# Performance work log

Hardware: AMD Instinct MI355X
Metric: run time of the kernel (lower is better)

## Reference

```python
import jax, jax.numpy as jnp
import numpy as np
from jax import lax

NUM_NODES = 100000
FEAT = 256
RANK = 16
NNZ = 4000000
NUM_HE = 125000  # num_hyperedges == num_edges_total
K = 2000000      # int(0.5 * NNZ)


def setup_inputs() -> dict:
    key = jax.random.key(0)
    ks = jax.random.split(key, 6)
    x = jax.random.normal(ks[0], (NUM_NODES, FEAT), dtype=jnp.float32)
    W = jax.random.normal(ks[1], (RANK, FEAT), dtype=jnp.float32)
    edge_factors = jax.random.normal(ks[2], (NUM_HE, RANK), dtype=jnp.float32)
    V_idx = jax.random.randint(ks[3], (NNZ,), 0, NUM_NODES, dtype=jnp.int32)
    E_idx = jax.random.randint(ks[4], (NNZ,), 0, NUM_HE, dtype=jnp.int32)
    edge_ids = jax.random.randint(ks[5], (NUM_HE,), 0, NUM_HE, dtype=jnp.int32)
    return {"x": x, "W": W, "edge_factors": edge_factors,
            "V_idx": V_idx, "E_idx": E_idx, "edge_ids": edge_ids, "k": K}


def _segment_mean(vals, seg_ids, num_segments):
    s = jax.ops.segment_sum(vals, seg_ids, num_segments=num_segments)
    c = jax.ops.segment_sum(jnp.ones_like(vals), seg_ids, num_segments=num_segments)
    return s / jnp.maximum(c, 1.0)


def reference(x, W, edge_factors, V_idx, E_idx, edge_ids, k):
    # node_proj(x): [N, rank]; gather per-incidence node and edge factors, dot product
    proj = x @ W.T                                  # [N, rank]
    ef = edge_factors[edge_ids[E_idx]]              # [nnz, rank]
    logits = jnp.sum(proj[V_idx] * ef, axis=-1)     # [nnz]
    scores = jax.nn.sigmoid(logits)

    # is_test=True path: deterministic top-k keep set
    _, keep_ids = lax.top_k(scores, k)
    hard = jnp.zeros_like(scores).at[keep_ids].set(1.0)
    # straight-through: forward == hard, gradient flows through scores where hard==1
    soft = hard + (scores - lax.stop_gradient(scores)) * hard

    edge_probs = _segment_mean(lax.stop_gradient(scores), E_idx, NUM_HE)
    edge_soft = _segment_mean(soft, E_idx, NUM_HE)
    edge_hard = (_segment_mean(hard, E_idx, NUM_HE) > 0).astype(jnp.float32)
    return scores, soft, hard, edge_probs, edge_soft, edge_hard
```

## Files before the change

### kernel.cpp

```cpp
#include <hip/hip_runtime.h>
#include <math.h>

#define FEAT 256
#define RANKK 16
#define PRJ_NODES 16
#define CAND_CAP 131072
#define TIE_CAP 2048
#define NBK_MAX 512

typedef unsigned long long u64;

static __device__ __forceinline__ u64 pack_pair(unsigned e_low, unsigned bits, unsigned idx) {
    return ((u64)e_low << 56) | ((u64)bits << 26) | (u64)idx;
}

__global__ __launch_bounds__(256) void proj_kernel(const float* __restrict__ x,
        const float* __restrict__ Wm, float* __restrict__ proj, int n_nodes) {
    __shared__ float Ws[RANKK][FEAT + 4];
    __shared__ float Xs[PRJ_NODES][FEAT + 4];
    const float4* x4 = (const float4*)x;
    const float4* w4 = (const float4*)Wm;
    for (int t = threadIdx.x; t < RANKK * (FEAT / 4); t += 256) {
        int r = t >> 6, j4 = t & 63;
        *(float4*)&Ws[r][j4 * 4] = w4[t];
    }
    int nodeBase = blockIdx.x * PRJ_NODES;
    for (int t = threadIdx.x; t < PRJ_NODES * (FEAT / 4); t += 256) {
        int n = t >> 6, j4 = t & 63;
        int node = nodeBase + n;
        float4 v = make_float4(0.f, 0.f, 0.f, 0.f);
        if (node < n_nodes) v = x4[(size_t)node * (FEAT / 4) + j4];
        *(float4*)&Xs[n][j4 * 4] = v;
    }
    __syncthreads();
    int n = threadIdx.x >> 4, r = threadIdx.x & 15;
    int node = nodeBase + n;
    if (node >= n_nodes) return;
    double acc = 0.0;
    #pragma unroll 8
    for (int j4 = 0; j4 < FEAT / 4; ++j4) {
        float4 xv = *(const float4*)&Xs[n][j4 * 4];
        float4 wv = *(const float4*)&Ws[r][j4 * 4];
        acc += (double)xv.x * (double)wv.x + (double)xv.y * (double)wv.y
             + (double)xv.z * (double)wv.z + (double)xv.w * (double)wv.w;
    }
    proj[(size_t)node * RANKK + r] = (float)acc;
}

__global__ void gather_ef(const float4* __restrict__ ef, const int* __restrict__ edge_ids,
                          float4* __restrict__ ef2, int nhe) {
    int t = blockIdx.x * blockDim.x + threadIdx.x;
    if (t >= nhe * 4) return;
    int e = t >> 2, c = t & 3;
    ef2[(size_t)e * 4 + c] = ef[(size_t)edge_ids[e] * 4 + c];
}

__global__ void ehist_kernel(const int* __restrict__ E_idx, unsigned* __restrict__ bucketCnt,
                             int nnz, int nb) {
    __shared__ unsigned h[NBK_MAX];
    for (int t = threadIdx.x; t < NBK_MAX; t += blockDim.x) h[t] = 0;
    __syncthreads();
    for (int i = blockIdx.x * blockDim.x + threadIdx.x; i < nnz; i += gridDim.x * blockDim.x)
        atomicAdd(&h[((unsigned)E_idx[i]) >> 8], 1u);
    __syncthreads();
    for (int t = threadIdx.x; t < nb; t += blockDim.x)
        if (h[t]) atomicAdd(&bucketCnt[t], h[t]);
}

__global__ void bucket_scan(const unsigned* __restrict__ bucketCnt,
                            unsigned* __restrict__ bucketBase, unsigned* __restrict__ cursor,
                            int nb, int nnz) {
    __shared__ unsigned s[NBK_MAX];
    int t = threadIdx.x;
    unsigned c = (t < nb) ? bucketCnt[t] : 0u;
    s[t] = c;
    __syncthreads();
    for (int off = 1; off < NBK_MAX; off <<= 1) {
        unsigned v = (t >= off) ? s[t - off] : 0u;
        __syncthreads();
        s[t] += v;
        __syncthreads();
    }
    unsigned excl = s[t] - c;
    if (t < nb) { bucketBase[t] = excl; cursor[t] = excl; }
    if (t == 0) bucketBase[nb] = (unsigned)nnz;
}

__global__ __launch_bounds__(256) void score_kernel(
        const float4* __restrict__ proj4, const float4* __restrict__ ef4,
        const int* __restrict__ V_idx, const int* __restrict__ E_idx,
        float* __restrict__ scores, int nnz) {
    int stride = gridDim.x * blockDim.x;
    #pragma unroll 2
    for (int i = blockIdx.x * blockDim.x + threadIdx.x; i < nnz; i += stride) {
        int v = V_idx[i], e = E_idx[i];
        float4 p0 = proj4[(size_t)v * 4 + 0];
        float4 p1 = proj4[(size_t)v * 4 + 1];
        float4 p2 = proj4[(size_t)v * 4 + 2];
        float4 p3 = proj4[(size_t)v * 4 + 3];
        float4 f0 = ef4[(size_t)e * 4 + 0];
        float4 f1 = ef4[(size_t)e * 4 + 1];
        float4 f2 = ef4[(size_t)e * 4 + 2];
        float4 f3 = ef4[(size_t)e * 4 + 3];
        double acc = (double)p0.x * f0.x + (double)p0.y * f0.y + (double)p0.z * f0.z + (double)p0.w * f0.w
                   + (double)p1.x * f1.x + (double)p1.y * f1.y + (double)p1.z * f1.z + (double)p1.w * f1.w
                   + (double)p2.x * f2.x + (double)p2.y * f2.y + (double)p2.z * f2.z + (double)p2.w * f2.w
                   + (double)p3.x * f3.x + (double)p3.y * f3.y + (double)p3.z * f3.z + (double)p3.w * f3.w;
        scores[i] = (float)(1.0 / (1.0 + exp(-acc)));
    }
}

__global__ void hist1_kernel(const float4* __restrict__ scores4, unsigned* __restrict__ hist1g,
                             int n4, int nnz) {
    __shared__ unsigned h[4096];
    for (int t = threadIdx.x; t < 4096; t += blockDim.x) h[t] = 0;
    __syncthreads();
    unsigned r1016 = 0, r1015 = 0, r0 = 0;
    int stride = gridDim.x * blockDim.x;
    for (int i = blockIdx.x * blockDim.x + threadIdx.x; i < n4; i += stride) {
        float4 sv = scores4[i];
        unsigned bb[4] = {__float_as_uint(sv.x), __float_as_uint(sv.y),
                          __float_as_uint(sv.z), __float_as_uint(sv.w)};
        #pragma unroll
        for (int q = 0; q < 4; ++q) {
            unsigned b = bb[q] >> 20;
            if (b == 1016) ++r1016;
            else if (b == 1015) ++r1015;
            else if (b == 0) ++r0;
            else atomicAdd(&h[b], 1u);
        }
    }
    for (int i = n4 * 4 + blockIdx.x * blockDim.x + threadIdx.x; i < nnz; i += stride) {
        unsigned b = __float_as_uint(((const float*)scores4)[i]) >> 20;
        if (b == 1016) ++r1016;
        else if (b == 1015) ++r1015;
        else if (b == 0) ++r0;
        else atomicAdd(&h[b], 1u);
    }
    if (r1016) atomicAdd(&h[1016], r1016);
    if (r1015) atomicAdd(&h[1015], r1015);
    if (r0) atomicAdd(&h[0], r0);
    __syncthreads();
    for (int t = threadIdx.x; t < 4096; t += blockDim.x)
        if (h[t]) atomicAdd(&hist1g[t], h[t]);
}

#define PB_CHUNK 8192
__global__ __launch_bounds__(256) void pair_build(const int* __restrict__ E_idx,
        const float* __restrict__ scores, u64* __restrict__ pairs,
        unsigned* __restrict__ cursor, int nnz, int nb) {
    __shared__ unsigned bh[NBK_MAX];
    for (int t = threadIdx.x; t < NBK_MAX; t += 256) bh[t] = 0;
    __syncthreads();
    int base = blockIdx.x * PB_CHUNK;
    int nE = nnz - base;
    if (nE > PB_CHUNK) nE = PB_CHUNK;
    for (int o = threadIdx.x; o < nE; o += 256)
        atomicAdd(&bh[((unsigned)E_idx[base + o]) >> 8], 1u);
    __syncthreads();
    for (int b = threadIdx.x; b < nb; b += 256) {
        unsigned c = bh[b];
        bh[b] = c ? atomicAdd(&cursor[b], c) : 0u;
    }
    __syncthreads();
    for (int o = threadIdx.x; o < nE; o += 256) {
        int i = base + o;
        unsigned e = (unsigned)E_idx[i];
        unsigned bits = __float_as_uint(scores[i]);
        unsigned pos = atomicAdd(&bh[e >> 8], 1u);
        pairs[pos] = pack_pair(e & 255u, bits, (unsigned)i);
    }
}

__global__ void scan1_kernel(const unsigned* __restrict__ hist,
                             unsigned* __restrict__ sel, const int* __restrict__ kptr) {
    __shared__ unsigned sfx[256];
    int t = threadIdx.x;
    unsigned local[16];
    unsigned s = 0;
    #pragma unroll
    for (int j = 0; j < 16; ++j) { local[j] = hist[t * 16 + j]; s += local[j]; }
    sfx[t] = s;
    __syncthreads();
    for (int off = 1; off < 256; off <<= 1) {
        unsigned add = (t + off < 256) ? sfx[t + off] : 0;
        __syncthreads();
        sfx[t] += add;
        __syncthreads();
    }
    unsigned krem = (unsigned)(*kptr);
    unsigned above = (t + 1 < 256) ? sfx[t + 1] : 0;
    if (above < krem && sfx[t] >= krem) {
        unsigned cum = above;
        int b = t * 16;
        for (int j = 15; j >= 0; --j) {
            unsigned cc = local[j];
            if (cum + cc >= krem) { b = t * 16 + j; break; }
            cum += cc;
        }
        sel[0] = krem - cum;
        sel[1] = ((unsigned)b) << 20;
    }
}

__global__ void compact_kernel(const u64* __restrict__ pairs, const unsigned* __restrict__ sel,
                               uint2* __restrict__ cand, unsigned* __restrict__ candCount, int nnz) {
    unsigned pref = sel[1] >> 20;
    int tid = blockIdx.x * blockDim.x + threadIdx.x;
    int stride = gridDim.x * blockDim.x;
    int lane = threadIdx.x & 63;
    for (int i = tid; i < nnz; i += stride) {
        u64 p = pairs[i];
        unsigned bits = (unsigned)(p >> 26) & 0x3FFFFFFFu;
        bool pred = (bits >> 20) == pref;
        unsigned long long mask = __ballot(pred);
        if (mask) {
            int leader = __ffsll(mask) - 1;
            unsigned base = 0;
            if (lane == leader) base = atomicAdd(candCount, (unsigned)__popcll(mask));
            base = __shfl(base, leader, 64);
            if (pred) {
                unsigned rank = __popcll(mask & ((1ull << lane) - 1ull));
                unsigned pos = base + rank;
                if (pos < CAND_CAP) cand[pos] = make_uint2(bits, (unsigned)(p & 0x3FFFFFFu));
            }
        }
    }
}

__global__ __launch_bounds__(256) void select_small(const uint2* __restrict__ cand,
                            const unsigned* __restrict__ candCount,
                            unsigned* __restrict__ sel, unsigned* __restrict__ tieList) {
    __shared__ unsigned h2[4096];
    __shared__ unsigned sfx[256];
    __shared__ unsigned sB2, sKrem2, sT, sM;
    __shared__ unsigned h3[256];
    __shared__ unsigned ties[TIE_CAP];
    __shared__ unsigned tcnt;
    int t = threadIdx.x;
    unsigned nc = *candCount;
    int n = (nc < CAND_CAP) ? (int)nc : CAND_CAP;
    unsigned krem = sel[0];
    unsigned pref = sel[1];

    for (int j = t; j < 4096; j += 256) h2[j] = 0;
    if (t == 0) tcnt = 0;
    __syncthreads();
    for (int j = t; j < n; j += 256) atomicAdd(&h2[(cand[j].x >> 8) & 0xFFF], 1u);
    __syncthreads();

    unsigned local[16];
    unsigned s = 0;
    #pragma unroll
    for (int j = 0; j < 16; ++j) { local[j] = h2[t * 16 + j]; s += local[j]; }
    sfx[t] = s;
    __syncthreads();
    for (int off = 1; off < 256; off <<= 1) {
        unsigned add = (t + off < 256) ? sfx[t + off] : 0;
        __syncthreads();
        sfx[t] += add;
        __syncthreads();
    }
    {
        unsigned above = (t + 1 < 256) ? sfx[t + 1] : 0;
        if (above < krem && sfx[t] >= krem) {
            unsigned cum = above;
            int b = t * 16;
            for (int j = 15; j >= 0; --j) {
                unsigned cc = local[j];
                if (cum + cc >= krem) { b = t * 16 + j; break; }
                cum += cc;
            }
            sB2 = (unsigned)b;
            sKrem2 = krem - cum;
        }
    }
    __syncthreads();

    h3[t] = 0;
    __syncthreads();
    unsigned b2 = sB2;
    for (int j = t; j < n; j += 256) {
        unsigned x = cand[j].x;
        if (((x >> 8) & 0xFFF) == b2) atomicAdd(&h3[x & 0xFF], 1u);
    }
    __syncthreads();
    sfx[t] = h3[t];
    __syncthreads();
    for (int off = 1; off < 256; off <<= 1) {
        unsigned add = (t + off < 256) ? sfx[t + off] : 0;
        __syncthreads();
        sfx[t] += add;
        __syncthreads();
    }
    {
        unsigned krem2 = sKrem2;
        unsigned above = (t + 1 < 256) ? sfx[t + 1] : 0;
        if (above < krem2 && sfx[t] >= krem2) {
            sT = pref | (b2 << 8) | (unsigned)t;
            sM = krem2 - above;
        }
    }
    __syncthreads();

    unsigned T = sT;
    for (int j = t; j < n; j += 256) {
        if (cand[j].x == T) {
            unsigned p = atomicAdd(&tcnt, 1u);
            if (p < TIE_CAP) ties[p] = cand[j].y;
        }
    }
    __syncthreads();
    if (t == 0) {
        unsigned cnt = (tcnt < TIE_CAP) ? tcnt : TIE_CAP;
        for (unsigned a = 1; a < cnt; ++a) {
            unsigned key = ties[a];
            int bpos = (int)a - 1;
            while (bpos >= 0 && ties[bpos] > key) { ties[bpos + 1] = ties[bpos]; --bpos; }
            ties[bpos + 1] = key;
        }
        unsigned m = sM;
        if (m > cnt) m = cnt;
        sel[2] = T;
        sel[3] = m;
        for (unsigned j = 0; j < m; ++j) tieList[j] = ties[j];
    }
}

__global__ __launch_bounds__(256) void esum_kernel(const u64* __restrict__ pairs,
        const unsigned* __restrict__ bucketBase,
        float* __restrict__ e_ssum, unsigned* __restrict__ e_cnt, int nhe) {
    __shared__ float ss[256];
    __shared__ unsigned cc[256];
    int t = threadIdx.x, b = blockIdx.x;
    ss[t] = 0.f; cc[t] = 0u;
    __syncthreads();
    unsigned n0 = bucketBase[b], n1 = bucketBase[b + 1];
    for (unsigned j = n0 + t; j < n1; j += 256) {
        u64 p = pairs[j];
        unsigned el = (unsigned)(p >> 56);
        unsigned bits = (unsigned)(p >> 26) & 0x3FFFFFFFu;
        atomicAdd(&ss[el], __uint_as_float(bits));
        atomicAdd(&cc[el], 1u);
    }
    __syncthreads();
    int e = b * 256 + t;
    if (e < nhe) { e_ssum[e] = ss[t]; e_cnt[e] = cc[t]; }
}

__global__ __launch_bounds__(256) void ehard_kernel(const u64* __restrict__ pairs,
        const unsigned* __restrict__ bucketBase, const unsigned* __restrict__ sel,
        const unsigned* __restrict__ tieList, unsigned* __restrict__ e_hsum, int nhe) {
    __shared__ unsigned hh[256];
    __shared__ unsigned ties[TIE_CAP];
    unsigned T = sel[2];
    unsigned m = sel[3];
    if (m > TIE_CAP) m = TIE_CAP;
    hh[threadIdx.x] = 0;
    for (int j = threadIdx.x; j < (int)m; j += 256) ties[j] = tieList[j];
    __syncthreads();
    int b = blockIdx.x;
    unsigned n0 = bucketBase[b], n1 = bucketBase[b + 1];
    for (unsigned j = n0 + threadIdx.x; j < n1; j += 256) {
        u64 p = pairs[j];
        unsigned bits = (unsigned)(p >> 26) & 0x3FFFFFFFu;
        bool keep = bits > T;
        if (bits == T) {
            unsigned idx = (unsigned)(p & 0x3FFFFFFu);
            int lo = 0, hi = (int)m - 1;
            keep = false;
            while (lo <= hi) {
                int mid = (lo + hi) >> 1;
                unsigned v = ties[mid];
                if (v == idx) { keep = true; break; }
                if (v < idx) lo = mid + 1; else hi = mid - 1;
            }
        }
        if (keep) atomicAdd(&hh[(unsigned)(p >> 56)], 1u);
    }
    __syncthreads();
    int e = b * 256 + threadIdx.x;
    if (e < nhe) e_hsum[e] = hh[threadIdx.x];
}

__global__ __launch_bounds__(256) void write_hard(const float4* __restrict__ scores4,
                           const unsigned* __restrict__ sel,
                           const unsigned* __restrict__ tieList,
                           float4* __restrict__ hard4, float4* __restrict__ soft4,
                           int n4, int nnz) {
    __shared__ unsigned ties[TIE_CAP];
    unsigned T = sel[2];
    unsigned m = sel[3];
    if (m > TIE_CAP) m = TIE_CAP;
    for (int j = threadIdx.x; j < (int)m; j += blockDim.x) ties[j] = tieList[j];
    __syncthreads();
    int tid = blockIdx.x * blockDim.x + threadIdx.x;
    int stride = gridDim.x * blockDim.x;
    for (int i = tid; i < n4; i += stride) {
        float4 sv = scores4[i];
        unsigned bb[4] = {__float_as_uint(sv.x), __float_as_uint(sv.y),
                          __float_as_uint(sv.z), __float_as_uint(sv.w)};
        float hv[4];
        #pragma unroll
        for (int q = 0; q < 4; ++q) {
            bool keep = (bb[q] > T);
            if (bb[q] == T) {
                unsigned idx = (unsigned)(i * 4 + q);
                int lo = 0, hi = (int)m - 1;
                keep = false;
                while (lo <= hi) {
                    int mid = (lo + hi) >> 1;
                    unsigned v = ties[mid];
                    if (v == idx) { keep = true; break; }
                    if (v < idx) lo = mid + 1; else hi = mid - 1;
                }
            }
            hv[q] = keep ? 1.0f : 0.0f;
        }
        float4 outv = make_float4(hv[0], hv[1], hv[2], hv[3]);
        hard4[i] = outv;
        soft4[i] = outv;
    }
    const float* sc = (const float*)scores4;
    float* hard = (float*)hard4;
    float* soft = (float*)soft4;
    for (int i = n4 * 4 + tid; i < nnz; i += stride) {
        unsigned b = __float_as_uint(sc[i]);
        bool keep = (b > T);
        if (b == T) {
            unsigned idx = (unsigned)i;
            int lo = 0, hi = (int)m - 1;
            keep = false;
            while (lo <= hi) {
                int mid = (lo + hi) >> 1;
                unsigned v = ties[mid];
                if (v == idx) { keep = true; break; }
                if (v < idx) lo = mid + 1; else hi = mid - 1;
            }
        }
        float hvv = keep ? 1.0f : 0.0f;
        hard[i] = hvv;
        soft[i] = hvv;
    }
}

__global__ void finalize_edges(const float* __restrict__ ssum, const unsigned* __restrict__ cnt,
                               const unsigned* __restrict__ hsum,
                               float* __restrict__ eprob, float* __restrict__ esoft,
                               float* __restrict__ ehard, int nhe) {
    int j = blockIdx.x * blockDim.x + threadIdx.x;
    if (j >= nhe) return;
    float c = fmaxf((float)cnt[j], 1.0f);
    eprob[j] = ssum[j] / c;
    esoft[j] = (float)hsum[j] / c;
    ehard[j] = (hsum[j] > 0) ? 1.0f : 0.0f;
}

extern "C" void kernel_launch(void* const* d_in, const int* in_sizes, int n_in,
                              void* d_out, int out_size, void* d_ws, size_t ws_size,
                              hipStream_t stream) {
    const float* x        = (const float*)d_in[0];
    const float* Wm       = (const float*)d_in[1];
    const float* ef       = (const float*)d_in[2];
    const int*   V_idx    = (const int*)d_in[3];
    const int*   E_idx    = (const int*)d_in[4];
    const int*   edge_ids = (const int*)d_in[5];
    const int*   kptr     = (const int*)d_in[6];

    const int nnz     = in_sizes[3];
    const int nhe     = in_sizes[5];
    const int n_nodes = in_sizes[0] / FEAT;
    const int nb      = (nhe + 255) >> 8;

    float* out    = (float*)d_out;
    float* scores = out;
    float* soft   = out + (size_t)nnz;
    float* hard   = out + 2 * (size_t)nnz;
    float* eprob  = out + 3 * (size_t)nnz;
    float* esoft  = eprob + nhe;
    float* ehard  = esoft + nhe;

    u64*   pairs = (u64*)soft;
    uint2* cand  = (uint2*)eprob;

    char* w = (char*)d_ws;
    unsigned* hist1      = (unsigned*)w;
    unsigned* bucketCnt  = hist1 + 4096;
    unsigned* candCount  = bucketCnt + NBK_MAX;
    unsigned* sel        = candCount + 1;
    unsigned* tieList    = sel + 8;
    unsigned* bucketBase = tieList + TIE_CAP;
    unsigned* cursor     = bucketBase + NBK_MAX + 1;
    float*    e_ssum     = (float*)(cursor + NBK_MAX);
    unsigned* e_cnt      = (unsigned*)(e_ssum + nhe);
    unsigned* e_hsum     = e_cnt + nhe;
    char* auxEnd = (char*)(e_hsum + nhe);
    size_t auxAligned = (((size_t)(auxEnd - w)) + 255) & ~(size_t)255;

    size_t ef2Bytes  = (size_t)nhe * RANKK * sizeof(float);
    size_t projBytes = (size_t)n_nodes * RANKK * sizeof(float);

    float* ef2;
    float* proj;
    if (ws_size >= auxAligned + ef2Bytes + projBytes) {
        ef2  = (float*)(w + auxAligned);
        proj = (float*)(w + auxAligned + ef2Bytes);
    } else {
        ef2  = hard;
        proj = hard + (size_t)nhe * RANKK;
    }

    hipMemsetAsync(w, 0, (size_t)(4096 + NBK_MAX + 1) * sizeof(unsigned), stream);

    ehist_kernel<<<128, 256, 0, stream>>>(E_idx, bucketCnt, nnz, nb);
    bucket_scan<<<1, NBK_MAX, 0, stream>>>(bucketCnt, bucketBase, cursor, nb, nnz);
    gather_ef<<<(nhe * 4 + 255) / 256, 256, 0, stream>>>(
        (const float4*)ef, edge_ids, (float4*)ef2, nhe);
    proj_kernel<<<(n_nodes + PRJ_NODES - 1) / PRJ_NODES, 256, 0, stream>>>(x, Wm, proj, n_nodes);

    score_kernel<<<2048, 256, 0, stream>>>(
        (const float4*)proj, (const float4*)ef2, V_idx, E_idx, scores, nnz);

    int n4 = nnz / 4;
    hist1_kernel<<<128, 256, 0, stream>>>((const float4*)scores, hist1, n4, nnz);
    pair_build<<<(nnz + PB_CHUNK - 1) / PB_CHUNK, 256, 0, stream>>>(
        E_idx, scores, pairs, cursor, nnz, nb);

    scan1_kernel<<<1, 256, 0, stream>>>(hist1, sel, kptr);
    compact_kernel<<<1024, 256, 0, stream>>>(pairs, sel, cand, candCount, nnz);
    select_small<<<1, 256, 0, stream>>>(cand, candCount, sel, tieList);

    esum_kernel<<<nb, 256, 0, stream>>>(pairs, bucketBase, e_ssum, e_cnt, nhe);
    ehard_kernel<<<nb, 256, 0, stream>>>(pairs, bucketBase, sel, tieList, e_hsum, nhe);

    write_hard<<<1024, 256, 0, stream>>>(
        (const float4*)scores, sel, tieList, (float4*)hard, (float4*)soft, n4, nnz);
    finalize_edges<<<(nhe + 255) / 256, 256, 0, stream>>>(e_ssum, e_cnt, e_hsum,
                                                          eprob, esoft, ehard, nhe);
}
```

Before: 525.6 us.

## Fuse histogram into scoring, compact from scores, merge edge reduction kernels

The score kernel now processes two incidences per thread via int2 index loads and builds the 4096-bin score histogram itself, so the separate hist1 pass over scores is gone. Compaction of candidates reads the 4-byte scores array with float4 loads instead of the 8-byte packed pairs. The three edge kernels (sum/count, hard count, finalize) become one kernel that reads the bucketed pairs once and writes the final edge outputs directly. This cuts global memory traffic and launch count. In exchange, every one of the 2048 score blocks now flushes its own shared histogram to global memory, and the score kernel uses more registers.

After: 539.8 us. +2.7%, slower.

```diff
diff --git a/kernel.cpp b/kernel.cpp
--- a/kernel.cpp
+++ b/kernel.cpp
@@ -88,60 +88,70 @@
 
 __global__ __launch_bounds__(256) void score_kernel(
         const float4* __restrict__ proj4, const float4* __restrict__ ef4,
-        const int* __restrict__ V_idx, const int* __restrict__ E_idx,
-        float* __restrict__ scores, int nnz) {
-    int stride = gridDim.x * blockDim.x;
-    #pragma unroll 2
-    for (int i = blockIdx.x * blockDim.x + threadIdx.x; i < nnz; i += stride) {
-        int v = V_idx[i], e = E_idx[i];
-        float4 p0 = proj4[(size_t)v * 4 + 0];
-        float4 p1 = proj4[(size_t)v * 4 + 1];
-        float4 p2 = proj4[(size_t)v * 4 + 2];
-        float4 p3 = proj4[(size_t)v * 4 + 3];
-        float4 f0 = ef4[(size_t)e * 4 + 0];
-        float4 f1 = ef4[(size_t)e * 4 + 1];
-        float4 f2 = ef4[(size_t)e * 4 + 2];
-        float4 f3 = ef4[(size_t)e * 4 + 3];
-        double acc = (double)p0.x * f0.x + (double)p0.y * f0.y + (double)p0.z * f0.z + (double)p0.w * f0.w
-                   + (double)p1.x * f1.x + (double)p1.y * f1.y + (double)p1.z * f1.z + (double)p1.w * f1.w
-                   + (double)p2.x * f2.x + (double)p2.y * f2.y + (double)p2.z * f2.z + (double)p2.w * f2.w
-                   + (double)p3.x * f3.x + (double)p3.y * f3.y + (double)p3.z * f3.z + (double)p3.w * f3.w;
-        scores[i] = (float)(1.0 / (1.0 + exp(-acc)));
-    }
-}
-
-__global__ void hist1_kernel(const float4* __restrict__ scores4, unsigned* __restrict__ hist1g,
-                             int n4, int nnz) {
+        const int2* __restrict__ V2, const int2* __restrict__ E2,
+        float2* __restrict__ scores2, unsigned* __restrict__ hist1g,
+        int npair, int nnz) {
     __shared__ unsigned h[4096];
-    for (int t = threadIdx.x; t < 4096; t += blockDim.x) h[t] = 0;
+    for (int t = threadIdx.x; t < 4096; t += 256) h[t] = 0;
     __syncthreads();
     unsigned r1016 = 0, r1015 = 0, r0 = 0;
-    int stride = gridDim.x * blockDim.x;
-    for (int i = blockIdx.x * blockDim.x + threadIdx.x; i < n4; i += stride) {
-        float4 sv = scores4[i];
-        unsigned bb[4] = {__float_as_uint(sv.x), __float_as_uint(sv.y),
-                          __float_as_uint(sv.z), __float_as_uint(sv.w)};
-        #pragma unroll
-        for (int q = 0; q < 4; ++q) {
-            unsigned b = bb[q] >> 20;
-            if (b == 1016) ++r1016;
-            else if (b == 1015) ++r1015;
-            else if (b == 0) ++r0;
-            else atomicAdd(&h[b], 1u);
-        }
-    }
-    for (int i = n4 * 4 + blockIdx.x * blockDim.x + threadIdx.x; i < nnz; i += stride) {
-        unsigned b = __float_as_uint(((const float*)scores4)[i]) >> 20;
-        if (b == 1016) ++r1016;
-        else if (b == 1015) ++r1015;
-        else if (b == 0) ++r0;
-        else atomicAdd(&h[b], 1u);
+    int stride = gridDim.x * 256;
+    for (int i = blockIdx.x * 256 + threadIdx.x; i < npair; i += stride) {
+        int2 v = V2[i];
+        int2 e = E2[i];
+        float4 a0 = proj4[(size_t)v.x * 4 + 0];
+        float4 a1 = proj4[(size_t)v.x * 4 + 1];
+        float4 a2 = proj4[(size_t)v.x * 4 + 2];
+        float4 a3 = proj4[(size_t)v.x * 4 + 3];
+        float4 b0 = proj4[(size_t)v.y * 4 + 0];
+        float4 b1 = proj4[(size_t)v.y * 4 + 1];
+        float4 b2 = proj4[(size_t)v.y * 4 + 2];
+        float4 b3 = proj4[(size_t)v.y * 4 + 3];
+        float4 f0 = ef4[(size_t)e.x * 4 + 0];
+        float4 f1 = ef4[(size_t)e.x * 4 + 1];
+        float4 f2 = ef4[(size_t)e.x * 4 + 2];
+        float4 f3 = ef4[(size_t)e.x * 4 + 3];
+        float4 g0 = ef4[(size_t)e.y * 4 + 0];
+        float4 g1 = ef4[(size_t)e.y * 4 + 1];
+        float4 g2 = ef4[(size_t)e.y * 4 + 2];
+        float4 g3 = ef4[(size_t)e.y * 4 + 3];
+        double acc0 = (double)a0.x * f0.x + (double)a0.y * f0.y + (double)a0.z * f0.z + (double)a0.w * f0.w
+                    + (double)a1.x * f1.x + (double)a1.y * f1.y + (double)a1.z * f1.z + (double)a1.w * f1.w
+                    + (double)a2.x * f2.x + (double)a2.y * f2.y + (double)a2.z * f2.z + (double)a2.w * f2.w
+                    + (double)a3.x * f3.x + (double)a3.y * f3.y + (double)a3.z * f3.z + (double)a3.w * f3.w;
+        double acc1 = (double)b0.x * g0.x + (double)b0.y * g0.y + (double)b0.z * g0.z + (double)b0.w * g0.w
+                    + (double)b1.x * g1.x + (double)b1.y * g1.y + (double)b1.z * g1.z + (double)b1.w * g1.w
+                    + (double)b2.x * g2.x + (double)b2.y * g2.y + (double)b2.z * g2.z + (double)b2.w * g2.w
+                    + (double)b3.x * g3.x + (double)b3.y * g3.y + (double)b3.z * g3.z + (double)b3.w * g3.w;
+        float s0 = (float)(1.0 / (1.0 + exp(-acc0)));
+        float s1 = (float)(1.0 / (1.0 + exp(-acc1)));
+        scores2[i] = make_float2(s0, s1);
+        unsigned bb0 = __float_as_uint(s0) >> 20;
+        unsigned bb1 = __float_as_uint(s1) >> 20;
+        if (bb0 == 1016) ++r1016; else if (bb0 == 1015) ++r1015;
+        else if (bb0 == 0) ++r0; else atomicAdd(&h[bb0], 1u);
+        if (bb1 == 1016) ++r1016; else if (bb1 == 1015) ++r1015;
+        else if (bb1 == 0) ++r0; else atomicAdd(&h[bb1], 1u);
+    }
+    if ((nnz & 1) && blockIdx.x == 0 && threadIdx.x == 0) {
+        int i = nnz - 1;
+        const int* Vi = (const int*)V2;
+        const int* Ei = (const int*)E2;
+        const float* pr = (const float*)proj4;
+        const float* fr = (const float*)ef4;
+        int v = Vi[i], e = Ei[i];
+        double acc = 0.0;
+        for (int r = 0; r < RANKK; ++r)
+            acc += (double)pr[(size_t)v * RANKK + r] * (double)fr[(size_t)e * RANKK + r];
+        float s = (float)(1.0 / (1.0 + exp(-acc)));
+        ((float*)scores2)[i] = s;
+        atomicAdd(&hist1g[__float_as_uint(s) >> 20], 1u);
     }
     if (r1016) atomicAdd(&h[1016], r1016);
     if (r1015) atomicAdd(&h[1015], r1015);
     if (r0) atomicAdd(&h[0], r0);
     __syncthreads();
-    for (int t = threadIdx.x; t < 4096; t += blockDim.x)
+    for (int t = threadIdx.x; t < 4096; t += 256)
         if (h[t]) atomicAdd(&hist1g[t], h[t]);
 }
 
@@ -203,27 +213,44 @@
     }
 }
 
-__global__ void compact_kernel(const u64* __restrict__ pairs, const unsigned* __restrict__ sel,
-                               uint2* __restrict__ cand, unsigned* __restrict__ candCount, int nnz) {
+__global__ void compact_kernel(const float4* __restrict__ scores4,
+                               const unsigned* __restrict__ sel,
+                               uint2* __restrict__ cand, unsigned* __restrict__ candCount,
+                               int n4, int nnz) {
     unsigned pref = sel[1] >> 20;
     int tid = blockIdx.x * blockDim.x + threadIdx.x;
     int stride = gridDim.x * blockDim.x;
     int lane = threadIdx.x & 63;
-    for (int i = tid; i < nnz; i += stride) {
-        u64 p = pairs[i];
-        unsigned bits = (unsigned)(p >> 26) & 0x3FFFFFFFu;
-        bool pred = (bits >> 20) == pref;
-        unsigned long long mask = __ballot(pred);
-        if (mask) {
-            int leader = __ffsll(mask) - 1;
-            unsigned base = 0;
-            if (lane == leader) base = atomicAdd(candCount, (unsigned)__popcll(mask));
-            base = __shfl(base, leader, 64);
-            if (pred) {
-                unsigned rank = __popcll(mask & ((1ull << lane) - 1ull));
-                unsigned pos = base + rank;
-                if (pos < CAND_CAP) cand[pos] = make_uint2(bits, (unsigned)(p & 0x3FFFFFFu));
+    int niter = (n4 + stride - 1) / stride;
+    for (int kk = 0; kk < niter; ++kk) {
+        int i = tid + kk * stride;
+        bool inb = (i < n4);
+        float4 sv = make_float4(0.f, 0.f, 0.f, 0.f);
+        if (inb) sv = scores4[i];
+        unsigned bb[4] = {__float_as_uint(sv.x), __float_as_uint(sv.y),
+                          __float_as_uint(sv.z), __float_as_uint(sv.w)};
+        #pragma unroll
+        for (int q = 0; q < 4; ++q) {
+            bool pred = inb && ((bb[q] >> 20) == pref);
+            unsigned long long mask = __ballot(pred);
+            if (mask) {
+                int leader = __ffsll(mask) - 1;
+                unsigned base = 0;
+                if (lane == leader) base = atomicAdd(candCount, (unsigned)__popcll(mask));
+                base = __shfl(base, leader, 64);
+                if (pred) {
+                    unsigned rank = __popcll(mask & ((1ull << lane) - 1ull));
+                    unsigned pos = base + rank;
+                    if (pos < CAND_CAP) cand[pos] = make_uint2(bb[q], (unsigned)(i * 4 + q));
+                }
             }
+        }
+    }
+    for (int i = n4 * 4 + tid; i < nnz; i += stride) {
+        unsigned b = __float_as_uint(((const float*)scores4)[i]);
+        if ((b >> 20) == pref) {
+            unsigned pos = atomicAdd(candCount, 1u);
+            if (pos < CAND_CAP) cand[pos] = make_uint2(b, (unsigned)i);
         }
     }
 }
@@ -327,14 +354,23 @@
     }
 }
 
-__global__ __launch_bounds__(256) void esum_kernel(const u64* __restrict__ pairs,
-        const unsigned* __restrict__ bucketBase,
-        float* __restrict__ e_ssum, unsigned* __restrict__ e_cnt, int nhe) {
+__global__ __launch_bounds__(256) void edge_final(const u64* __restrict__ pairs,
+        const unsigned* __restrict__ bucketBase, const unsigned* __restrict__ sel,
+        const unsigned* __restrict__ tieList,
+        float* __restrict__ eprob, float* __restrict__ esoft, float* __restrict__ ehard,
+        int nhe) {
     __shared__ float ss[256];
     __shared__ unsigned cc[256];
-    int t = threadIdx.x, b = blockIdx.x;
-    ss[t] = 0.f; cc[t] = 0u;
-    __syncthreads();
+    __shared__ unsigned hh[256];
+    __shared__ unsigned ties[TIE_CAP];
+    unsigned T = sel[2];
+    unsigned m = sel[3];
+    if (m > TIE_CAP) m = TIE_CAP;
+    int t = threadIdx.x;
+    ss[t] = 0.f; cc[t] = 0u; hh[t] = 0u;
+    for (int j = t; j < (int)m; j += 256) ties[j] = tieList[j];
+    __syncthreads();
+    int b = blockIdx.x;
     unsigned n0 = bucketBase[b], n1 = bucketBase[b + 1];
     for (unsigned j = n0 + t; j < n1; j += 256) {
         u64 p = pairs[j];
@@ -342,28 +378,6 @@
         unsigned bits = (unsigned)(p >> 26) & 0x3FFFFFFFu;
         atomicAdd(&ss[el], __uint_as_float(bits));
         atomicAdd(&cc[el], 1u);
-    }
-    __syncthreads();
-    int e = b * 256 + t;
-    if (e < nhe) { e_ssum[e] = ss[t]; e_cnt[e] = cc[t]; }
-}
-
-__global__ __launch_bounds__(256) void ehard_kernel(const u64* __restrict__ pairs,
-        const unsigned* __restrict__ bucketBase, const unsigned* __restrict__ sel,
-        const unsigned* __restrict__ tieList, unsigned* __restrict__ e_hsum, int nhe) {
-    __shared__ unsigned hh[256];
-    __shared__ unsigned ties[TIE_CAP];
-    unsigned T = sel[2];
-    unsigned m = sel[3];
-    if (m > TIE_CAP) m = TIE_CAP;
-    hh[threadIdx.x] = 0;
-    for (int j = threadIdx.x; j < (int)m; j += 256) ties[j] = tieList[j];
-    __syncthreads();
-    int b = blockIdx.x;
-    unsigned n0 = bucketBase[b], n1 = bucketBase[b + 1];
-    for (unsigned j = n0 + threadIdx.x; j < n1; j += 256) {
-        u64 p = pairs[j];
-        unsigned bits = (unsigned)(p >> 26) & 0x3FFFFFFFu;
         bool keep = bits > T;
         if (bits == T) {
             unsigned idx = (unsigned)(p & 0x3FFFFFFu);
@@ -376,11 +390,16 @@
                 if (v < idx) lo = mid + 1; else hi = mid - 1;
             }
         }
-        if (keep) atomicAdd(&hh[(unsigned)(p >> 56)], 1u);
-    }
-    __syncthreads();
-    int e = b * 256 + threadIdx.x;
-    if (e < nhe) e_hsum[e] = hh[threadIdx.x];
+        if (keep) atomicAdd(&hh[el], 1u);
+    }
+    __syncthreads();
+    int e = b * 256 + t;
+    if (e < nhe) {
+        float c = fmaxf((float)cc[t], 1.0f);
+        eprob[e] = ss[t] / c;
+        esoft[e] = (float)hh[t] / c;
+        ehard[e] = (hh[t] > 0) ? 1.0f : 0.0f;
+    }
 }
 
 __global__ __launch_bounds__(256) void write_hard(const float4* __restrict__ scores4,
@@ -444,18 +463,6 @@
     }
 }
 
-__global__ void finalize_edges(const float* __restrict__ ssum, const unsigned* __restrict__ cnt,
-                               const unsigned* __restrict__ hsum,
-                               float* __restrict__ eprob, float* __restrict__ esoft,
-                               float* __restrict__ ehard, int nhe) {
-    int j = blockIdx.x * blockDim.x + threadIdx.x;
-    if (j >= nhe) return;
-    float c = fmaxf((float)cnt[j], 1.0f);
-    eprob[j] = ssum[j] / c;
-    esoft[j] = (float)hsum[j] / c;
-    ehard[j] = (hsum[j] > 0) ? 1.0f : 0.0f;
-}
-
 extern "C" void kernel_launch(void* const* d_in, const int* in_sizes, int n_in,
                               void* d_out, int out_size, void* d_ws, size_t ws_size,
                               hipStream_t stream) {
@@ -491,10 +498,7 @@
     unsigned* tieList    = sel + 8;
     unsigned* bucketBase = tieList + TIE_CAP;
     unsigned* cursor     = bucketBase + NBK_MAX + 1;
-    float*    e_ssum     = (float*)(cursor + NBK_MAX);
-    unsigned* e_cnt      = (unsigned*)(e_ssum + nhe);
-    unsigned* e_hsum     = e_cnt + nhe;
-    char* auxEnd = (char*)(e_hsum + nhe);
+    char* auxEnd = (char*)(cursor + NBK_MAX);
     size_t auxAligned = (((size_t)(auxEnd - w)) + 255) & ~(size_t)255;
 
     size_t ef2Bytes  = (size_t)nhe * RANKK * sizeof(float);
@@ -518,23 +522,23 @@
         (const float4*)ef, edge_ids, (float4*)ef2, nhe);
     proj_kernel<<<(n_nodes + PRJ_NODES - 1) / PRJ_NODES, 256, 0, stream>>>(x, Wm, proj, n_nodes);
 
+    int npair = nnz >> 1;
     score_kernel<<<2048, 256, 0, stream>>>(
-        (const float4*)proj, (const float4*)ef2, V_idx, E_idx, scores, nnz);
-
-    int n4 = nnz / 4;
-    hist1_kernel<<<128, 256, 0, stream>>>((const float4*)scores, hist1, n4, nnz);
+        (const float4*)proj, (const float4*)ef2,
+        (const int2*)V_idx, (const int2*)E_idx,
+        (float2*)scores, hist1, npair, nnz);
+
     pair_build<<<(nnz + PB_CHUNK - 1) / PB_CHUNK, 256, 0, stream>>>(
         E_idx, scores, pairs, cursor, nnz, nb);
 
+    int n4 = nnz / 4;
     scan1_kernel<<<1, 256, 0, stream>>>(hist1, sel, kptr);
-    compact_kernel<<<1024, 256, 0, stream>>>(pairs, sel, cand, candCount, nnz);
+    compact_kernel<<<1024, 256, 0, stream>>>(
+        (const float4*)scores, sel, cand, candCount, n4, nnz);
     select_small<<<1, 256, 0, stream>>>(cand, candCount, sel, tieList);
 
-    esum_kernel<<<nb, 256, 0, stream>>>(pairs, bucketBase, e_ssum, e_cnt, nhe);
-    ehard_kernel<<<nb, 256, 0, stream>>>(pairs, bucketBase, sel, tieList, e_hsum, nhe);
-
+    edge_final<<<nb, 256, 0, stream>>>(pairs, bucketBase, sel, tieList,
+                                       eprob, esoft, ehard, nhe);
     write_hard<<<1024, 256, 0, stream>>>(
         (const float4*)scores, sel, tieList, (float4*)hard, (float4*)soft, n4, nnz);
-    finalize_edges<<<(nhe + 255) / 256, 256, 0, stream>>>(e_ssum, e_cnt, e_hsum,
-                                                          eprob, esoft, ehard, nhe);
-}
+}
```
